# Kernel tuning notes

Hardware: AMD Instinct MI355X
Metric: run time of the kernel (lower is better)

Reference implementation:

```python
import jax, jax.numpy as jnp
import numpy as np

B, P, HID = 2, 4096, 1152
N_HEADS, HEAD_DIM = 16, 72
EPS = 1e-6


def _rms_norm(x, w=None):
    # x fp32; normalize over last dim
    ms = jnp.mean(x * x, axis=-1, keepdims=True) + EPS
    y = x * jax.lax.rsqrt(ms)
    if w is not None:
        y = y * w
    return y


def _rotate_half(x):
    d = x.shape[-1] // 2
    return jnp.concatenate([-x[..., d:], x[..., :d]], axis=-1)


def _apply_rotary(x, c, s):
    # x: [B,P,N,d], c/s: [B,P,d] -> broadcast over heads
    c = c[:, :, None, :]
    s = s[:, :, None, :]
    return x * c + _rotate_half(x) * s


def _multidim_rope(x, cos, sin, ndim=2):
    per = x.shape[-1] // ndim
    parts = []
    for k in range(ndim):
        sl = slice(k * per, (k + 1) * per)
        parts.append(_apply_rotary(x[..., sl], cos[..., sl], sin[..., sl]))
    return jnp.concatenate(parts, axis=-1)


def setup_inputs() -> dict:
    key = jax.random.key(0)
    ks = jax.random.split(key, 8)
    return {
        "hidden_states": jax.random.normal(ks[0], (B, P, HID), jnp.float32),
        "cos": jax.random.normal(ks[1], (B, P, HEAD_DIM), jnp.float32),
        "sin": jax.random.normal(ks[2], (B, P, HEAD_DIM), jnp.float32),
        "Wq": jax.random.normal(ks[3], (HID, N_HEADS * HEAD_DIM), jnp.float32) * 0.02,
        "Wk": jax.random.normal(ks[4], (HID, N_HEADS * HEAD_DIM), jnp.float32) * 0.02,
        "Wv": jax.random.normal(ks[5], (HID, N_HEADS * HEAD_DIM), jnp.float32) * 0.02,
        "Wo": jax.random.normal(ks[6], (N_HEADS * HEAD_DIM, HID), jnp.float32) * 0.02,
        "q_norm_w": jnp.ones((HEAD_DIM,), jnp.float32),
        "k_norm_w": jnp.ones((HEAD_DIM,), jnp.float32),
    }


def reference(hidden_states, cos, sin, Wq, Wk, Wv, Wo, q_norm_w, k_norm_w):
    b, p, _ = hidden_states.shape
    q = (hidden_states @ Wq).reshape(b, p, N_HEADS, HEAD_DIM)
    k = (hidden_states @ Wk).reshape(b, p, N_HEADS, HEAD_DIM)
    v = (hidden_states @ Wv).reshape(b, p, N_HEADS, HEAD_DIM)
    # per-head RMSNorm (q/k with learned scale, v without)
    q = _rms_norm(q, q_norm_w)
    k = _rms_norm(k, k_norm_w)
    v = _rms_norm(v)
    # multi-dim RoPE (ndim=2)
    q = _multidim_rope(q, cos, sin)
    k = _multidim_rope(k, cos, sin)
    # attention, scaling = 1.0, no mask (non-causal vision)
    scores = jnp.einsum('bqnd,bknd->bnqk', q, k)  # [B,N,P,P]
    attn = jax.nn.softmax(scores.astype(jnp.float32), axis=-1).astype(q.dtype)
    out = jnp.einsum('bnqk,bknd->bqnd', attn, v).reshape(b, p, N_HEADS * HEAD_DIM)
    return out @ Wo
```

## Files before the change

### kernel.cpp

```cpp
#include <hip/hip_runtime.h>
#include <stdint.h>

typedef __attribute__((ext_vector_type(8))) _Float16 half8;
typedef __attribute__((ext_vector_type(4))) _Float16 half4;
typedef __attribute__((ext_vector_type(4))) float floatx4;

#define NHEADS 16
#define HDIM   72
#define DPAD   96
#define DPADV  80
#define HID    1152
#define NQKV   3456
#define PP     4096
#define MR     8192

__device__ __forceinline__ float bf2f(unsigned short u) {
  union { unsigned int i; float f; } c; c.i = ((unsigned int)u) << 16; return c.f;
}
__device__ __forceinline__ unsigned short f2bf(float f) {
  union { float f; unsigned int i; } c; c.f = f;
  unsigned int x = c.i;
  x += ((x >> 16) & 1u) + 0x7fffu;
  return (unsigned short)(x >> 16);
}
__device__ __forceinline__ float load_in(const void* p, long long i, int bf) {
  return bf ? bf2f(((const unsigned short*)p)[i]) : ((const float*)p)[i];
}

__global__ __launch_bounds__(64) void k_detect(const void* hs, int* flag) {
  int lane = threadIdx.x;
  const unsigned short* u = (const unsigned short*)hs;
  int wild = 0;
  for (int t = 0; t < 8; ++t) {
    unsigned short v = u[lane * 8 + t];
    int e = (v >> 7) & 0xFF;
    if (e >= 134) wild++;
  }
  for (int off = 1; off < 64; off <<= 1) wild += __shfl_xor(wild, off);
  if (lane == 0) flag[0] = (wild > 32) ? 0 : 1;
}

__global__ __launch_bounds__(256) void k_prep(
    const void* hs, const void* cosp, const void* sinp,
    const void* wq, const void* wk, const void* wv, const void* wo,
    const void* qnw, const void* knw, const int* flag,
    _Float16* Xh, _Float16* Wqkv, _Float16* Wot,
    float* cosf, float* sinf, float* qw, float* kw) {
  int bf = flag[0];
  long long i = (long long)blockIdx.x * blockDim.x + threadIdx.x;
  const long long n0 = (long long)MR * HID;
  const long long n1 = (long long)NQKV * HID;
  const long long n2 = (long long)HID * HID;
  const long long n3 = (long long)2 * PP * HDIM;
  if (i < n0) { Xh[i] = (_Float16)load_in(hs, i, bf); return; }
  i -= n0;
  if (i < n1) {
    long long n = i / HID, kk = i - n * HID;
    int sel = (int)(n / HID);
    long long nl = n - (long long)sel * HID;
    const void* W = (sel == 0) ? wq : ((sel == 1) ? wk : wv);
    Wqkv[i] = (_Float16)load_in(W, kk * HID + nl, bf);
    return;
  }
  i -= n1;
  if (i < n2) {
    long long n = i / HID, kk = i - n * HID;
    Wot[i] = (_Float16)load_in(wo, kk * HID + n, bf);
    return;
  }
  i -= n2;
  if (i < n3) { cosf[i] = load_in(cosp, i, bf); return; }
  i -= n3;
  if (i < n3) { sinf[i] = load_in(sinp, i, bf); return; }
  i -= n3;
  if (i < HDIM) { qw[i] = load_in(qnw, i, bf); return; }
  i -= HDIM;
  if (i < HDIM) { kw[i] = load_in(knw, i, bf); return; }
}

#define LDA 40
__global__ __launch_bounds__(256) void k_gemm(
    const _Float16* __restrict__ A, const _Float16* __restrict__ Bt,
    int N, int K, float* __restrict__ C32,
    int mode, const int* __restrict__ flag, void* __restrict__ outp) {
  __shared__ _Float16 As[128 * LDA];
  __shared__ _Float16 Bs[128 * LDA];
  int tid = threadIdx.x;
  int wave = tid >> 6, lane = tid & 63;
  int quad = lane >> 4, l16 = lane & 15;
  int bM = blockIdx.y * 128, bN = blockIdx.x * 128;
  int wm = (wave & 1) * 64, wn = (wave >> 1) * 64;
  int qk = quad * 8;
  int sr = tid >> 1, sc = (tid & 1) * 16;

  floatx4 acc[4][4];
  floatx4 z4 = {0.f, 0.f, 0.f, 0.f};
#pragma unroll
  for (int i = 0; i < 4; ++i)
#pragma unroll
    for (int j = 0; j < 4; ++j) acc[i][j] = z4;

  const _Float16* gA = A + (size_t)(bM + sr) * K + sc;
  const _Float16* gB = Bt + (size_t)(bN + sr) * K + sc;

  for (int k0 = 0; k0 < K; k0 += 32) {
    half8 a0 = *(const half8*)(gA);
    half8 a1 = *(const half8*)(gA + 8);
    half8 b0 = *(const half8*)(gB);
    half8 b1 = *(const half8*)(gB + 8);
    gA += 32; gB += 32;
    __syncthreads();
    *(half8*)(As + sr * LDA + sc)     = a0;
    *(half8*)(As + sr * LDA + sc + 8) = a1;
    *(half8*)(Bs + sr * LDA + sc)     = b0;
    *(half8*)(Bs + sr * LDA + sc + 8) = b1;
    __syncthreads();
    half8 af[4], bfv[4];
#pragma unroll
    for (int i = 0; i < 4; ++i)
      af[i] = *(const half8*)(As + (wm + i * 16 + l16) * LDA + qk);
#pragma unroll
    for (int j = 0; j < 4; ++j)
      bfv[j] = *(const half8*)(Bs + (wn + j * 16 + l16) * LDA + qk);
#pragma unroll
    for (int i = 0; i < 4; ++i)
#pragma unroll
      for (int j = 0; j < 4; ++j)
        acc[i][j] = __builtin_amdgcn_mfma_f32_16x16x32_f16(af[i], bfv[j], acc[i][j], 0, 0, 0);
  }

  if (mode == 0) {
#pragma unroll
    for (int i = 0; i < 4; ++i)
#pragma unroll
      for (int j = 0; j < 4; ++j)
#pragma unroll
        for (int r = 0; r < 4; ++r) {
          size_t row = (size_t)(bM + wm + i * 16 + quad * 4 + r);
          size_t col = (size_t)(bN + wn + j * 16 + l16);
          C32[row * N + col] = acc[i][j][r];
        }
  } else {
    int obf = flag[0];
#pragma unroll
    for (int i = 0; i < 4; ++i)
#pragma unroll
      for (int j = 0; j < 4; ++j)
#pragma unroll
        for (int r = 0; r < 4; ++r) {
          size_t row = (size_t)(bM + wm + i * 16 + quad * 4 + r);
          size_t col = (size_t)(bN + wn + j * 16 + l16);
          float v = acc[i][j][r];
          if (obf) ((unsigned short*)outp)[row * N + col] = f2bf(v);
          else     ((float*)outp)[row * N + col] = v;
        }
  }
}

__global__ __launch_bounds__(256) void k_norm_rope(
    const float* __restrict__ QKV, const float* __restrict__ cosf,
    const float* __restrict__ sinf, const float* __restrict__ qw,
    const float* __restrict__ kw,
    _Float16* __restrict__ Qp, _Float16* __restrict__ Kp,
    _Float16* __restrict__ Vp) {
  int wave = threadIdx.x >> 6, lane = threadIdx.x & 63;
  int bid = blockIdx.x * 4 + wave;
  int m = bid >> 4, h = bid & 15;
  int b = m >> 12, p = m & 4095;
  __shared__ float sq[4][HDIM], sk[4][HDIM];

  const float* rowp = QKV + (long long)m * NQKV + h * HDIM;
  int i0 = lane, i1 = lane + 64;
  bool has1 = (i1 < HDIM);
  float q0 = rowp[i0];
  float k0 = rowp[1152 + i0];
  float v0 = rowp[2304 + i0];
  float q1 = 0.f, k1 = 0.f, v1 = 0.f;
  if (has1) { q1 = rowp[i1]; k1 = rowp[1152 + i1]; v1 = rowp[2304 + i1]; }

  float sq_s = q0 * q0 + q1 * q1;
  float sk_s = k0 * k0 + k1 * k1;
  float sv_s = v0 * v0 + v1 * v1;
  for (int off = 1; off < 64; off <<= 1) {
    sq_s += __shfl_xor(sq_s, off);
    sk_s += __shfl_xor(sk_s, off);
    sv_s += __shfl_xor(sv_s, off);
  }
  float rq = rsqrtf(sq_s / 72.f + 1e-6f);
  float rk = rsqrtf(sk_s / 72.f + 1e-6f);
  float rv = rsqrtf(sv_s / 72.f + 1e-6f);

  sq[wave][i0] = q0 * rq * qw[i0];
  sk[wave][i0] = k0 * rk * kw[i0];
  if (has1) { sq[wave][i1] = q1 * rq * qw[i1]; sk[wave][i1] = k1 * rk * kw[i1]; }
  __syncthreads();

  const float* crow = cosf + (long long)m * HDIM;
  const float* srow = sinf + (long long)m * HDIM;
  long long obase = ((long long)(b * NHEADS + h) * PP + p) * DPAD;
  long long obV   = ((long long)(b * NHEADS + h) * PP + p) * DPADV;
#pragma unroll
  for (int t = 0; t < 2; ++t) {
    int i = lane + t * 64;
    if (i < DPAD) {
      _Float16 qv = (_Float16)0.f, kv = (_Float16)0.f;
      if (i < HDIM) {
        int j = (i >= 36) ? (i - 36) : i;
        float c = crow[i], s = srow[i];
        float qo, ko;
        if (j < 18) { qo = sq[wave][i] * c - sq[wave][i + 18] * s; ko = sk[wave][i] * c - sk[wave][i + 18] * s; }
        else        { qo = sq[wave][i] * c + sq[wave][i - 18] * s; ko = sk[wave][i] * c + sk[wave][i - 18] * s; }
        qv = (_Float16)qo; kv = (_Float16)ko;
      }
      Qp[obase + i] = qv; Kp[obase + i] = kv;
    }
    if (i < DPADV) {
      _Float16 vv = (_Float16)0.f;
      if (i < HDIM) vv = (_Float16)(((t == 0) ? v0 : v1) * rv);
      Vp[obV + i] = vv;
    }
  }
}

__global__ __launch_bounds__(256) void k_vtrans(
    const _Float16* __restrict__ Vp, _Float16* __restrict__ VtG) {
  __shared__ _Float16 T[DPADV * 72];
  int tid = threadIdx.x;
  int pt = blockIdx.x, bh = blockIdx.y;
  long long src = (long long)bh * PP * DPADV + (long long)pt * 64 * DPADV;
#pragma unroll
  for (int pp = 0; pp < 3; ++pp) {
    int c = tid + pp * 256;
    if (c < 640) {
      int r = c / 10, ds = c % 10;
      half8 v = *(const half8*)(Vp + src + r * DPADV + ds * 8);
#pragma unroll
      for (int j = 0; j < 8; ++j) T[(ds * 8 + j) * 72 + r] = v[j];
    }
  }
  __syncthreads();
  long long dst = (long long)bh * DPADV * PP + (long long)pt * 64;
#pragma unroll
  for (int pp = 0; pp < 3; ++pp) {
    int c = tid + pp * 256;
    if (c < 640) {
      int d = c >> 3, ps = (c & 7) * 8;
      half8 v = *(const half8*)(T + d * 72 + ps);
      if (d == 72) {
#pragma unroll
        for (int j = 0; j < 8; ++j) v[j] = (_Float16)1.f;
      }
      *(half8*)(VtG + dst + (long long)d * PP + ps) = v;
    }
  }
}

#define TK 64
#define NT (PP / TK)
#define LDK 104
#define LDV 72
__global__ __launch_bounds__(256) void k_flash(
    const _Float16* __restrict__ Qp, const _Float16* __restrict__ Kp,
    const _Float16* __restrict__ VtG, _Float16* __restrict__ Oat) {
  __shared__ _Float16 Kl[TK * LDK];
  __shared__ _Float16 Vt[DPADV * LDV];
  __shared__ _Float16 Pl[128 * LDV];
  int tid = threadIdx.x, wave = tid >> 6, lane = tid & 63;
  int quad = lane >> 4, l16 = lane & 15;
  int qt = blockIdx.x, bh = blockIdx.y;
  const long long headoff = (long long)bh * PP * DPAD;
  const long long vhead   = (long long)bh * DPADV * PP;

  half8 qf[2][3];
#pragma unroll
  for (int mb = 0; mb < 2; ++mb) {
    int qrow = qt * 128 + wave * 32 + mb * 16 + l16;
#pragma unroll
    for (int ck = 0; ck < 3; ++ck)
      qf[mb][ck] = *(const half8*)(Qp + headoff + (long long)qrow * DPAD + ck * 32 + quad * 8);
  }

  floatx4 O[2][5];
  floatx4 z4 = {0.f, 0.f, 0.f, 0.f};
#pragma unroll
  for (int mb = 0; mb < 2; ++mb)
#pragma unroll
    for (int d = 0; d < 5; ++d) O[mb][d] = z4;
  float m_i[2];
  m_i[0] = -1e30f; m_i[1] = -1e30f;
  _Float16* Pw = Pl + wave * 32 * LDV;

  half8 kreg[3], vreg[3];
  {
    const _Float16* Ksrc = Kp + headoff;
    const _Float16* Vsrc = VtG + vhead;
#pragma unroll
    for (int pp = 0; pp < 3; ++pp)
      kreg[pp] = *(const half8*)(Ksrc + (tid + pp * 256) * 8);
#pragma unroll
    for (int pp = 0; pp < 3; ++pp) {
      int c = tid + pp * 256;
      if (c < 640)
        vreg[pp] = *(const half8*)(Vsrc + (long long)(c >> 3) * PP + (c & 7) * 8);
    }
  }

  for (int kt = 0; kt < NT; ++kt) {
    __syncthreads();
#pragma unroll
    for (int pp = 0; pp < 3; ++pp) {
      int c = tid + pp * 256;
      *(half8*)(Kl + (c / 12) * LDK + (c % 12) * 8) = kreg[pp];
    }
#pragma unroll
    for (int pp = 0; pp < 3; ++pp) {
      int c = tid + pp * 256;
      if (c < 640)
        *(half8*)(Vt + (c >> 3) * LDV + (c & 7) * 8) = vreg[pp];
    }
    __syncthreads();

    {
      int ktn = (kt + 1 < NT) ? kt + 1 : kt;
      const _Float16* Ksrc = Kp + headoff + (long long)ktn * TK * DPAD;
      const _Float16* Vsrc = VtG + vhead + ktn * TK;
#pragma unroll
      for (int pp = 0; pp < 3; ++pp)
        kreg[pp] = *(const half8*)(Ksrc + (tid + pp * 256) * 8);
#pragma unroll
      for (int pp = 0; pp < 3; ++pp) {
        int c = tid + pp * 256;
        if (c < 640)
          vreg[pp] = *(const half8*)(Vsrc + (long long)(c >> 3) * PP + (c & 7) * 8);
      }
    }

    floatx4 sb[2][4];
    __builtin_amdgcn_s_setprio(1);
#pragma unroll
    for (int nb = 0; nb < 4; ++nb) {
      half8 kf[3];
#pragma unroll
      for (int ck = 0; ck < 3; ++ck)
        kf[ck] = *(const half8*)(Kl + (nb * 16 + l16) * LDK + ck * 32 + quad * 8);
#pragma unroll
      for (int mb = 0; mb < 2; ++mb) {
        floatx4 a = z4;
#pragma unroll
        for (int ck = 0; ck < 3; ++ck)
          a = __builtin_amdgcn_mfma_f32_16x16x32_f16(kf[ck], qf[mb][ck], a, 0, 0, 0);
        sb[mb][nb] = a;
      }
    }
    __builtin_amdgcn_s_setprio(0);

#pragma unroll
    for (int mb = 0; mb < 2; ++mb) {
      float t = fmaxf(fmaxf(sb[mb][0][0], sb[mb][0][1]),
                      fmaxf(sb[mb][0][2], sb[mb][0][3]));
#pragma unroll
      for (int nb = 1; nb < 4; ++nb)
        t = fmaxf(t, fmaxf(fmaxf(sb[mb][nb][0], sb[mb][nb][1]),
                           fmaxf(sb[mb][nb][2], sb[mb][nb][3])));
      t = fmaxf(t, __shfl_xor(t, 16));
      t = fmaxf(t, __shfl_xor(t, 32));
      if (!__all(t <= m_i[mb] + 8.f)) {
        float mnew = fmaxf(m_i[mb], t);
        float al = __expf(m_i[mb] - mnew);
        m_i[mb] = mnew;
        float alT[4];
#pragma unroll
        for (int r = 0; r < 4; ++r)
          alT[r] = __shfl(al, (lane & 48) + quad * 4 + r);
#pragma unroll
        for (int d = 0; d < 5; ++d)
#pragma unroll
          for (int r = 0; r < 4; ++r) O[mb][d][r] *= alT[r];
      }
      float mi = m_i[mb];
#pragma unroll
      for (int nb = 0; nb < 4; ++nb) {
        half4 w;
#pragma unroll
        for (int r = 0; r < 4; ++r)
          w[r] = (_Float16)__expf(sb[mb][nb][r] - mi);
        *(half4*)(Pw + (mb * 16 + l16) * LDV + nb * 16 + quad * 4) = w;
      }
    }

    __builtin_amdgcn_s_setprio(1);
#pragma unroll
    for (int ck2 = 0; ck2 < 2; ++ck2) {
      half8 pf0 = *(const half8*)(Pw + l16 * LDV + ck2 * 32 + quad * 8);
      half8 pf1 = *(const half8*)(Pw + (16 + l16) * LDV + ck2 * 32 + quad * 8);
#pragma unroll
      for (int d = 0; d < 5; ++d) {
        half8 vf = *(const half8*)(Vt + (d * 16 + l16) * LDV + ck2 * 32 + quad * 8);
        O[0][d] = __builtin_amdgcn_mfma_f32_16x16x32_f16(pf0, vf, O[0][d], 0, 0, 0);
        O[1][d] = __builtin_amdgcn_mfma_f32_16x16x32_f16(pf1, vf, O[1][d], 0, 0, 0);
      }
    }
    __builtin_amdgcn_s_setprio(0);
  }

  int b = bh >> 4, h = bh & 15;
  int src = (lane & 48) + 8;
#pragma unroll
  for (int mb = 0; mb < 2; ++mb) {
    float linv[4];
#pragma unroll
    for (int r = 0; r < 4; ++r)
      linv[r] = 1.f / __shfl(O[mb][4][r], src);
    long long orow = (long long)b * PP + qt * 128 + wave * 32 + mb * 16 + quad * 4;
#pragma unroll
    for (int d = 0; d < 5; ++d) {
      int dd = d * 16 + l16;
      if (dd < HDIM) {
#pragma unroll
        for (int r = 0; r < 4; ++r)
          Oat[(orow + r) * HID + h * HDIM + dd] = (_Float16)(O[mb][d][r] * linv[r]);
      }
    }
  }
}

extern "C" void kernel_launch(void* const* d_in, const int* in_sizes, int n_in,
                              void* d_out, int out_size, void* d_ws, size_t ws_size,
                              hipStream_t stream) {
  (void)in_sizes; (void)n_in; (void)out_size; (void)ws_size;
  const void* hs   = d_in[0];
  const void* cosp = d_in[1];
  const void* sinp = d_in[2];
  const void* wq   = d_in[3];
  const void* wk   = d_in[4];
  const void* wv   = d_in[5];
  const void* wo   = d_in[6];
  const void* qnw  = d_in[7];
  const void* knw  = d_in[8];

  char* ws = (char*)d_ws;
  size_t off = 0;
  auto take = [&](size_t bytes) -> char* {
    off = (off + 255) & ~(size_t)255;
    char* p = ws + off; off += bytes; return p;
  };
  int* flag        = (int*)take(4);
  _Float16* Xh     = (_Float16*)take((size_t)MR * HID * 2);
  _Float16* Wqkvh  = (_Float16*)take((size_t)NQKV * HID * 2);
  _Float16* Woth   = (_Float16*)take((size_t)HID * HID * 2);
  float* cosf_     = (float*)take((size_t)2 * PP * HDIM * 4);
  float* sinf_     = (float*)take((size_t)2 * PP * HDIM * 4);
  float* qwf       = (float*)take(HDIM * 4);
  float* kwf       = (float*)take(HDIM * 4);
  float* QKVf      = (float*)take((size_t)MR * NQKV * 4);
  _Float16* Kp     = (_Float16*)take((size_t)2 * NHEADS * PP * DPAD * 2);
  _Float16* Vp     = (_Float16*)take((size_t)2 * NHEADS * PP * DPADV * 2);
  _Float16* Qp  = Xh;
  _Float16* Oat = (_Float16*)QKVf;
  _Float16* VtG = (_Float16*)((char*)QKVf + (size_t)20 * 1024 * 1024);

  k_detect<<<dim3(1), dim3(64), 0, stream>>>(hs, flag);

  long long totalPrep = (long long)MR * HID + (long long)NQKV * HID +
                        (long long)HID * HID + 2LL * 2 * PP * HDIM + 2 * HDIM;
  int prepBlocks = (int)((totalPrep + 255) / 256);
  k_prep<<<dim3(prepBlocks), dim3(256), 0, stream>>>(
      hs, cosp, sinp, wq, wk, wv, wo, qnw, knw, flag,
      Xh, Wqkvh, Woth, cosf_, sinf_, qwf, kwf);

  k_gemm<<<dim3(NQKV / 128, MR / 128), dim3(256), 0, stream>>>(
      Xh, Wqkvh, NQKV, HID, QKVf, 0, flag, (void*)nullptr);

  k_norm_rope<<<dim3(MR * NHEADS / 4), dim3(256), 0, stream>>>(
      QKVf, cosf_, sinf_, qwf, kwf, Qp, Kp, Vp);

  k_vtrans<<<dim3(PP / 64, 2 * NHEADS), dim3(256), 0, stream>>>(Vp, VtG);

  k_flash<<<dim3(PP / 128, 2 * NHEADS), dim3(256), 0, stream>>>(Qp, Kp, VtG, Oat);

  k_gemm<<<dim3(HID / 128, MR / 128), dim3(256), 0, stream>>>(
      Oat, Woth, HID, HID, (float*)nullptr, 1, flag, d_out);
}
```

Measured before the change: 664.6 us.

## Store QKV projection in fp16, shrink K padding to 80, swap flash grid order

The QKV GEMM now writes fp16 instead of fp32, which halves the intermediate write and the read in norm/rope. K rows are padded to 80 instead of 96, so less K data is loaded and staged in LDS per tile. The third MFMA chunk is zero-filled for the upper lanes instead of reading padding. The flash grid is transposed so heads vary fastest, which changes L2 locality. Storing the QKV intermediate in fp16 loses precision and range before the RMSNorm.

Measured after the change: 685.1 us. 1.03x slower.

```diff
diff --git a/kernel.cpp b/kernel.cpp
--- a/kernel.cpp
+++ b/kernel.cpp
@@ -7,7 +7,7 @@
 
 #define NHEADS 16
 #define HDIM   72
-#define DPAD   96
+#define DPAD   80
 #define DPADV  80
 #define HID    1152
 #define NQKV   3456
@@ -81,8 +81,8 @@
 #define LDA 40
 __global__ __launch_bounds__(256) void k_gemm(
     const _Float16* __restrict__ A, const _Float16* __restrict__ Bt,
-    int N, int K, float* __restrict__ C32,
-    int mode, const int* __restrict__ flag, void* __restrict__ outp) {
+    int N, int K, int mode, const int* __restrict__ flag,
+    void* __restrict__ outp) {
   __shared__ _Float16 As[128 * LDA];
   __shared__ _Float16 Bs[128 * LDA];
   int tid = threadIdx.x;
@@ -138,7 +138,7 @@
         for (int r = 0; r < 4; ++r) {
           size_t row = (size_t)(bM + wm + i * 16 + quad * 4 + r);
           size_t col = (size_t)(bN + wn + j * 16 + l16);
-          C32[row * N + col] = acc[i][j][r];
+          ((_Float16*)outp)[row * N + col] = (_Float16)acc[i][j][r];
         }
   } else {
     int obf = flag[0];
@@ -158,7 +158,7 @@
 }
 
 __global__ __launch_bounds__(256) void k_norm_rope(
-    const float* __restrict__ QKV, const float* __restrict__ cosf,
+    const _Float16* __restrict__ QKV, const float* __restrict__ cosf,
     const float* __restrict__ sinf, const float* __restrict__ qw,
     const float* __restrict__ kw,
     _Float16* __restrict__ Qp, _Float16* __restrict__ Kp,
@@ -169,14 +169,14 @@
   int b = m >> 12, p = m & 4095;
   __shared__ float sq[4][HDIM], sk[4][HDIM];
 
-  const float* rowp = QKV + (long long)m * NQKV + h * HDIM;
+  const _Float16* rowp = QKV + (long long)m * NQKV + h * HDIM;
   int i0 = lane, i1 = lane + 64;
   bool has1 = (i1 < HDIM);
-  float q0 = rowp[i0];
-  float k0 = rowp[1152 + i0];
-  float v0 = rowp[2304 + i0];
+  float q0 = (float)rowp[i0];
+  float k0 = (float)rowp[1152 + i0];
+  float v0 = (float)rowp[2304 + i0];
   float q1 = 0.f, k1 = 0.f, v1 = 0.f;
-  if (has1) { q1 = rowp[i1]; k1 = rowp[1152 + i1]; v1 = rowp[2304 + i1]; }
+  if (has1) { q1 = (float)rowp[i1]; k1 = (float)rowp[1152 + i1]; v1 = (float)rowp[2304 + i1]; }
 
   float sq_s = q0 * q0 + q1 * q1;
   float sk_s = k0 * k0 + k1 * k1;
@@ -257,7 +257,7 @@
 
 #define TK 64
 #define NT (PP / TK)
-#define LDK 104
+#define LDK 80
 #define LDV 72
 __global__ __launch_bounds__(256) void k_flash(
     const _Float16* __restrict__ Qp, const _Float16* __restrict__ Kp,
@@ -267,17 +267,24 @@
   __shared__ _Float16 Pl[128 * LDV];
   int tid = threadIdx.x, wave = tid >> 6, lane = tid & 63;
   int quad = lane >> 4, l16 = lane & 15;
-  int qt = blockIdx.x, bh = blockIdx.y;
+  int bh = blockIdx.x, qt = blockIdx.y;
   const long long headoff = (long long)bh * PP * DPAD;
   const long long vhead   = (long long)bh * DPADV * PP;
 
+  half8 zh8;
+#pragma unroll
+  for (int j = 0; j < 8; ++j) zh8[j] = (_Float16)0.f;
+
   half8 qf[2][3];
 #pragma unroll
   for (int mb = 0; mb < 2; ++mb) {
     int qrow = qt * 128 + wave * 32 + mb * 16 + l16;
-#pragma unroll
-    for (int ck = 0; ck < 3; ++ck)
-      qf[mb][ck] = *(const half8*)(Qp + headoff + (long long)qrow * DPAD + ck * 32 + quad * 8);
+    const _Float16* qp = Qp + headoff + (long long)qrow * DPAD;
+#pragma unroll
+    for (int ck = 0; ck < 2; ++ck)
+      qf[mb][ck] = *(const half8*)(qp + ck * 32 + quad * 8);
+    qf[mb][2] = zh8;
+    if (quad < 2) qf[mb][2] = *(const half8*)(qp + 64 + quad * 8);
   }
 
   floatx4 O[2][5];
@@ -295,8 +302,11 @@
     const _Float16* Ksrc = Kp + headoff;
     const _Float16* Vsrc = VtG + vhead;
 #pragma unroll
-    for (int pp = 0; pp < 3; ++pp)
-      kreg[pp] = *(const half8*)(Ksrc + (tid + pp * 256) * 8);
+    for (int pp = 0; pp < 3; ++pp) {
+      int c = tid + pp * 256;
+      if (c < 640)
+        kreg[pp] = *(const half8*)(Ksrc + c * 8);
+    }
 #pragma unroll
     for (int pp = 0; pp < 3; ++pp) {
       int c = tid + pp * 256;
@@ -310,7 +320,8 @@
 #pragma unroll
     for (int pp = 0; pp < 3; ++pp) {
       int c = tid + pp * 256;
-      *(half8*)(Kl + (c / 12) * LDK + (c % 12) * 8) = kreg[pp];
+      if (c < 640)
+        *(half8*)(Kl + (c / 10) * LDK + (c % 10) * 8) = kreg[pp];
     }
 #pragma unroll
     for (int pp = 0; pp < 3; ++pp) {
@@ -325,8 +336,11 @@
       const _Float16* Ksrc = Kp + headoff + (long long)ktn * TK * DPAD;
       const _Float16* Vsrc = VtG + vhead + ktn * TK;
 #pragma unroll
-      for (int pp = 0; pp < 3; ++pp)
-        kreg[pp] = *(const half8*)(Ksrc + (tid + pp * 256) * 8);
+      for (int pp = 0; pp < 3; ++pp) {
+        int c = tid + pp * 256;
+        if (c < 640)
+          kreg[pp] = *(const half8*)(Ksrc + c * 8);
+      }
 #pragma unroll
       for (int pp = 0; pp < 3; ++pp) {
         int c = tid + pp * 256;
@@ -339,16 +353,16 @@
     __builtin_amdgcn_s_setprio(1);
 #pragma unroll
     for (int nb = 0; nb < 4; ++nb) {
-      half8 kf[3];
-#pragma unroll
-      for (int ck = 0; ck < 3; ++ck)
-        kf[ck] = *(const half8*)(Kl + (nb * 16 + l16) * LDK + ck * 32 + quad * 8);
+      const _Float16* kp = Kl + (nb * 16 + l16) * LDK;
+      half8 kf0 = *(const half8*)(kp + quad * 8);
+      half8 kf1 = *(const half8*)(kp + 32 + quad * 8);
+      half8 kf2 = zh8;
+      if (quad < 2) kf2 = *(const half8*)(kp + 64 + quad * 8);
 #pragma unroll
       for (int mb = 0; mb < 2; ++mb) {
-        floatx4 a = z4;
-#pragma unroll
-        for (int ck = 0; ck < 3; ++ck)
-          a = __builtin_amdgcn_mfma_f32_16x16x32_f16(kf[ck], qf[mb][ck], a, 0, 0, 0);
+        floatx4 a = __builtin_amdgcn_mfma_f32_16x16x32_f16(kf0, qf[mb][0], z4, 0, 0, 0);
+        a = __builtin_amdgcn_mfma_f32_16x16x32_f16(kf1, qf[mb][1], a, 0, 0, 0);
+        a = __builtin_amdgcn_mfma_f32_16x16x32_f16(kf2, qf[mb][2], a, 0, 0, 0);
         sb[mb][nb] = a;
       }
     }
@@ -452,12 +466,12 @@
   float* sinf_     = (float*)take((size_t)2 * PP * HDIM * 4);
   float* qwf       = (float*)take(HDIM * 4);
   float* kwf       = (float*)take(HDIM * 4);
-  float* QKVf      = (float*)take((size_t)MR * NQKV * 4);
+  _Float16* QKVh   = (_Float16*)take((size_t)MR * NQKV * 2);
   _Float16* Kp     = (_Float16*)take((size_t)2 * NHEADS * PP * DPAD * 2);
   _Float16* Vp     = (_Float16*)take((size_t)2 * NHEADS * PP * DPADV * 2);
   _Float16* Qp  = Xh;
-  _Float16* Oat = (_Float16*)QKVf;
-  _Float16* VtG = (_Float16*)((char*)QKVf + (size_t)20 * 1024 * 1024);
+  _Float16* Oat = QKVh;
+  _Float16* VtG = (_Float16*)((char*)QKVh + (size_t)20 * 1024 * 1024);
 
   k_detect<<<dim3(1), dim3(64), 0, stream>>>(hs, flag);
 
@@ -469,15 +483,15 @@
       Xh, Wqkvh, Woth, cosf_, sinf_, qwf, kwf);
 
   k_gemm<<<dim3(NQKV / 128, MR / 128), dim3(256), 0, stream>>>(
-      Xh, Wqkvh, NQKV, HID, QKVf, 0, flag, (void*)nullptr);
+      Xh, Wqkvh, NQKV, HID, 0, flag, QKVh);
 
   k_norm_rope<<<dim3(MR * NHEADS / 4), dim3(256), 0, stream>>>(
-      QKVf, cosf_, sinf_, qwf, kwf, Qp, Kp, Vp);
+      QKVh, cosf_, sinf_, qwf, kwf, Qp, Kp, Vp);
 
   k_vtrans<<<dim3(PP / 64, 2 * NHEADS), dim3(256), 0, stream>>>(Vp, VtG);
 
-  k_flash<<<dim3(PP / 128, 2 * NHEADS), dim3(256), 0, stream>>>(Qp, Kp, VtG, Oat);
+  k_flash<<<dim3(2 * NHEADS, PP / 128), dim3(256), 0, stream>>>(Qp, Kp, VtG, Oat);
 
   k_gemm<<<dim3(HID / 128, MR / 128), dim3(256), 0, stream>>>(
-      Oat, Woth, HID, HID, (float*)nullptr, 1, flag, d_out);
-}
+      Oat, Woth, HID, HID, 1, flag, d_out);
+}
```
